# Performance work log

Hardware: AMD Instinct MI355X
Metric: run time of the kernel (lower is better)

Reference implementation:

```python
import jax, jax.numpy as jnp
import numpy as np

EMBED_DIM = 256
B, S = 4, 8192


def setup_inputs() -> dict:
    key = jax.random.key(0)
    ks = jax.random.split(key, 9)
    d = EMBED_DIM
    s = 1.0 / np.sqrt(d)
    return {
        "x": jax.random.normal(ks[0], (B, S, d), dtype=jnp.float32),
        "Wq": jax.random.uniform(ks[1], (d, d), jnp.float32, -s, s),
        "bq": jax.random.uniform(ks[2], (d,), jnp.float32, -s, s),
        "Wk": jax.random.uniform(ks[3], (d, d), jnp.float32, -s, s),
        "bk": jax.random.uniform(ks[4], (d,), jnp.float32, -s, s),
        "Wv": jax.random.uniform(ks[5], (d, d), jnp.float32, -s, s),
        "bv": jax.random.uniform(ks[6], (d,), jnp.float32, -s, s),
        "Wo": jax.random.uniform(ks[7], (d, d), jnp.float32, -s, s),
        "bo": jax.random.uniform(ks[8], (d,), jnp.float32, -s, s),
    }


def reference(x, Wq, bq, Wk, bk, Wv, bv, Wo, bo):
    # Linear layers: y = x @ W^T + b (torch convention: W is [out, in])
    d = x.shape[-1]
    scaling = d ** (-0.5)
    q = x @ Wq.T + bq                       # [B, S, d]
    k = x @ Wk.T + bk
    v = x @ Wv.T + bv
    scores = jnp.einsum("bsd,btd->bst", q, k) * scaling  # [B, S, S]
    weights = jax.nn.softmax(scores, axis=-1)
    attn = jnp.einsum("bst,btd->bsd", weights, v)        # [B, S, d]
    return attn @ Wo.T + bo
```

## Files before the change

### kernel.cpp

```cpp
#include <hip/hip_runtime.h>
#include <hip/hip_bf16.h>

typedef __attribute__((ext_vector_type(8))) short short8;
typedef __attribute__((ext_vector_type(4))) float f32x4;

#define SEQ 8192
#define NBATCH 4
#define NT (SEQ / 32)

static __device__ __forceinline__ unsigned short f2bf(float f) {
    __hip_bfloat16 h = __float2bfloat16(f);
    unsigned short u;
    __builtin_memcpy(&u, &h, 2);
    return u;
}

static __device__ __forceinline__ int4 pack8(float4 a, float4 b) {
    union { unsigned short s[8]; int4 i; } r;
    r.s[0] = f2bf(a.x); r.s[1] = f2bf(a.y); r.s[2] = f2bf(a.z); r.s[3] = f2bf(a.w);
    r.s[4] = f2bf(b.x); r.s[5] = f2bf(b.y); r.s[6] = f2bf(b.z); r.s[7] = f2bf(b.w);
    return r.i;
}

template<bool A_BF16, int OMODE>
__global__ __launch_bounds__(256) void proj_gemm(
    const void* __restrict__ Ap, const float* __restrict__ W,
    const float* __restrict__ bias, void* __restrict__ Outp, float scale)
{
    __shared__ alignas(16) unsigned short As[128][40];
    __shared__ alignas(16) unsigned short Bs[128][40];

    const int tid  = threadIdx.x;
    const int lane = tid & 63;
    const int wv   = tid >> 6;
    const int wm   = (wv >> 1) * 64, wn = (wv & 1) * 64;
    const int lr   = lane & 15, lg = lane >> 4;
    const int m0   = blockIdx.x * 128;
    const int n0   = blockIdx.y * 128;

    const int srow = tid >> 1;
    const int skc  = (tid & 1) * 16;

    f32x4 acc[4][4] = {};

    for (int k0 = 0; k0 < 256; k0 += 32) {
        __syncthreads();
        if (A_BF16) {
            const unsigned short* a = (const unsigned short*)Ap + (size_t)(m0 + srow) * 256 + k0 + skc;
            int4 v0 = *(const int4*)a;
            int4 v1 = *(const int4*)(a + 8);
            *(int4*)&As[srow][skc]     = v0;
            *(int4*)&As[srow][skc + 8] = v1;
        } else {
            const float* a = (const float*)Ap + (size_t)(m0 + srow) * 256 + k0 + skc;
            const float4* a4 = (const float4*)a;
            *(int4*)&As[srow][skc]     = pack8(a4[0], a4[1]);
            *(int4*)&As[srow][skc + 8] = pack8(a4[2], a4[3]);
        }
        {
            const float* b = W + (size_t)(n0 + srow) * 256 + k0 + skc;
            const float4* b4 = (const float4*)b;
            *(int4*)&Bs[srow][skc]     = pack8(b4[0], b4[1]);
            *(int4*)&Bs[srow][skc + 8] = pack8(b4[2], b4[3]);
        }
        __syncthreads();

        short8 af[4], bfr[4];
        #pragma unroll
        for (int fm = 0; fm < 4; ++fm)
            af[fm] = *(const short8*)&As[wm + fm * 16 + lr][lg * 8];
        #pragma unroll
        for (int fn = 0; fn < 4; ++fn)
            bfr[fn] = *(const short8*)&Bs[wn + fn * 16 + lr][lg * 8];
        #pragma unroll
        for (int fm = 0; fm < 4; ++fm)
            #pragma unroll
            for (int fn = 0; fn < 4; ++fn)
                acc[fm][fn] = __builtin_amdgcn_mfma_f32_16x16x32_bf16(
                    af[fm], bfr[fn], acc[fm][fn], 0, 0, 0);
    }

    float bvals[4];
    #pragma unroll
    for (int fn = 0; fn < 4; ++fn) bvals[fn] = bias[n0 + wn + fn * 16 + lr];

    #pragma unroll
    for (int fm = 0; fm < 4; ++fm) {
        #pragma unroll
        for (int fn = 0; fn < 4; ++fn) {
            #pragma unroll
            for (int r = 0; r < 4; ++r) {
                const int row = m0 + wm + fm * 16 + lg * 4 + r;
                const int col = n0 + wn + fn * 16 + lr;
                float val = (acc[fm][fn][r] + bvals[fn]) * scale;
                if (OMODE == 1) {
                    ((float*)Outp)[(size_t)row * 256 + col] = val;
                } else if (OMODE == 0) {
                    ((unsigned short*)Outp)[(size_t)row * 256 + col] = f2bf(val);
                } else {
                    const int bb = row >> 13, s = row & 8191;
                    ((unsigned short*)Outp)[((size_t)(bb * 256 + col) << 13) + s] = f2bf(val);
                }
            }
        }
    }
}

__global__ __launch_bounds__(256) void attn_kernel(
    const unsigned short* __restrict__ Q, const unsigned short* __restrict__ K,
    const unsigned short* __restrict__ Vt, unsigned short* __restrict__ A)
{
    __shared__ alignas(16) unsigned short Ks[2][32][264];
    __shared__ alignas(16) unsigned short Ps[2][4][16][40];
    __shared__ alignas(16) float Cor[2][4][16];
    __shared__ alignas(16) float Ls[4][16];
    __shared__ int Flg[2][4];

    const int tid  = threadIdx.x;
    const int lane = tid & 63;
    const int wv   = tid >> 6;
    const int lr   = lane & 15, lg = lane >> 4;
    const int b    = blockIdx.y;
    const size_t qblk = (size_t)b * SEQ + blockIdx.x * 64;

    short8 aq[8];
    #pragma unroll
    for (int c = 0; c < 8; ++c)
        aq[c] = *(const short8*)&Q[(qblk + wv * 16 + lr) * 256 + c * 32 + lg * 8];

    float m_run = -1e30f, l_run = 0.f;
    f32x4 o[4][4] = {};

    const int krow = tid >> 3, kcol = (tid & 7) * 32;
    const unsigned short* Vb = Vt + ((size_t)b * 256 << 13);
    size_t vrow[4];
    #pragma unroll
    for (int dt = 0; dt < 4; ++dt)
        vrow[dt] = (size_t)(wv * 64 + dt * 16 + lr) << 13;

    {
        const int4* src = (const int4*)&K[((size_t)b * SEQ + krow) * 256 + kcol];
        int4 x0 = src[0], x1 = src[1], x2 = src[2], x3 = src[3];
        *(int4*)&Ks[0][krow][kcol]      = x0;
        *(int4*)&Ks[0][krow][kcol + 8]  = x1;
        *(int4*)&Ks[0][krow][kcol + 16] = x2;
        *(int4*)&Ks[0][krow][kcol + 24] = x3;
    }
    __syncthreads();

    for (int it = 0; it < NT; ++it) {
        const int p = it & 1;
        int4 x0, x1, x2, x3;
        const bool have = (it + 1 < NT);
        if (have) {
            const int4* src = (const int4*)&K[((size_t)b * SEQ + (it + 1) * 32 + krow) * 256 + kcol];
            x0 = src[0]; x1 = src[1]; x2 = src[2]; x3 = src[3];
        }
        short8 vbr[4];
        if (it > 0) {
            const size_t kvp = (size_t)(it - 1) * 32 + lg * 8;
            #pragma unroll
            for (int dt = 0; dt < 4; ++dt)
                vbr[dt] = *(const short8*)&Vb[vrow[dt] + kvp];
        }

        f32x4 s0 = {}, s1 = {};
        #pragma unroll
        for (int c = 0; c < 8; ++c) {
            short8 kb0 = *(const short8*)&Ks[p][lr][c * 32 + lg * 8];
            short8 kb1 = *(const short8*)&Ks[p][16 + lr][c * 32 + lg * 8];
            s0 = __builtin_amdgcn_mfma_f32_16x16x32_bf16(kb0, aq[c], s0, 0, 0, 0);
            s1 = __builtin_amdgcn_mfma_f32_16x16x32_bf16(kb1, aq[c], s1, 0, 0, 0);
        }

        if (have) {
            *(int4*)&Ks[p ^ 1][krow][kcol]      = x0;
            *(int4*)&Ks[p ^ 1][krow][kcol + 8]  = x1;
            *(int4*)&Ks[p ^ 1][krow][kcol + 16] = x2;
            *(int4*)&Ks[p ^ 1][krow][kcol + 24] = x3;
        }

        float mx = fmaxf(fmaxf(fmaxf(s0[0], s0[1]), fmaxf(s0[2], s0[3])),
                         fmaxf(fmaxf(s1[0], s1[1]), fmaxf(s1[2], s1[3])));
        mx = fmaxf(mx, __shfl_xor(mx, 16, 64));
        mx = fmaxf(mx, __shfl_xor(mx, 32, 64));

        const int need = __any(mx > m_run + 11.0f);
        float corr = 1.f;
        if (need) {
            float mnew = fmaxf(m_run, mx);
            corr = exp2f(m_run - mnew);
            m_run = mnew;
            if (lane < 16) Cor[p ^ 1][wv][lr] = corr;
        }
        if (lane == 0) Flg[p ^ 1][wv] = need;

        float p0[4], p1[4];
        #pragma unroll
        for (int r = 0; r < 4; ++r) {
            p0[r] = exp2f(s0[r] - m_run);
            p1[r] = exp2f(s1[r] - m_run);
        }
        float rs = ((p0[0] + p0[1]) + (p0[2] + p0[3])) +
                   ((p1[0] + p1[1]) + (p1[2] + p1[3]));
        rs += __shfl_xor(rs, 16, 64);
        rs += __shfl_xor(rs, 32, 64);
        l_run = (need ? l_run * corr : l_run) + rs;

        {
            unsigned int w0 = (unsigned)f2bf(p0[0]) | ((unsigned)f2bf(p0[1]) << 16);
            unsigned int w1 = (unsigned)f2bf(p0[2]) | ((unsigned)f2bf(p0[3]) << 16);
            unsigned int w2 = (unsigned)f2bf(p1[0]) | ((unsigned)f2bf(p1[1]) << 16);
            unsigned int w3 = (unsigned)f2bf(p1[2]) | ((unsigned)f2bf(p1[3]) << 16);
            *(unsigned long long*)&Ps[p ^ 1][wv][lr][4 * lg] =
                (unsigned long long)w0 | ((unsigned long long)w1 << 32);
            *(unsigned long long*)&Ps[p ^ 1][wv][lr][16 + 4 * lg] =
                (unsigned long long)w2 | ((unsigned long long)w3 << 32);
        }

        if (it > 0) {
            short8 pa[4];
            #pragma unroll
            for (int qt = 0; qt < 4; ++qt)
                pa[qt] = *(const short8*)&Ps[p][qt][lr][lg * 8];
            #pragma unroll
            for (int qt = 0; qt < 4; ++qt) {
                if (Flg[p][qt]) {
                    float4 c4 = *(const float4*)&Cor[p][qt][lg * 4];
                    #pragma unroll
                    for (int dt = 0; dt < 4; ++dt) {
                        o[qt][dt][0] *= c4.x; o[qt][dt][1] *= c4.y;
                        o[qt][dt][2] *= c4.z; o[qt][dt][3] *= c4.w;
                    }
                }
                #pragma unroll
                for (int dt = 0; dt < 4; ++dt)
                    o[qt][dt] = __builtin_amdgcn_mfma_f32_16x16x32_bf16(pa[qt], vbr[dt], o[qt][dt], 0, 0, 0);
            }
        }
        __syncthreads();
    }

    {
        const int p = NT & 1;
        const size_t kvp = (size_t)(NT - 1) * 32 + lg * 8;
        short8 vbr[4];
        #pragma unroll
        for (int dt = 0; dt < 4; ++dt)
            vbr[dt] = *(const short8*)&Vb[vrow[dt] + kvp];
        short8 pa[4];
        #pragma unroll
        for (int qt = 0; qt < 4; ++qt)
            pa[qt] = *(const short8*)&Ps[p][qt][lr][lg * 8];
        #pragma unroll
        for (int qt = 0; qt < 4; ++qt) {
            if (Flg[p][qt]) {
                float4 c4 = *(const float4*)&Cor[p][qt][lg * 4];
                #pragma unroll
                for (int dt = 0; dt < 4; ++dt) {
                    o[qt][dt][0] *= c4.x; o[qt][dt][1] *= c4.y;
                    o[qt][dt][2] *= c4.z; o[qt][dt][3] *= c4.w;
                }
            }
            #pragma unroll
            for (int dt = 0; dt < 4; ++dt)
                o[qt][dt] = __builtin_amdgcn_mfma_f32_16x16x32_bf16(pa[qt], vbr[dt], o[qt][dt], 0, 0, 0);
        }
    }

    if (lane < 16) Ls[wv][lr] = l_run;
    __syncthreads();
    #pragma unroll
    for (int qt = 0; qt < 4; ++qt) {
        float4 l4 = *(const float4*)&Ls[qt][lg * 4];
        float inv[4] = {1.f / l4.x, 1.f / l4.y, 1.f / l4.z, 1.f / l4.w};
        #pragma unroll
        for (int dt = 0; dt < 4; ++dt)
            #pragma unroll
            for (int r = 0; r < 4; ++r)
                A[(qblk + qt * 16 + lg * 4 + r) * 256 + wv * 64 + dt * 16 + lr] =
                    f2bf(o[qt][dt][r] * inv[r]);
    }
}

extern "C" void kernel_launch(void* const* d_in, const int* in_sizes, int n_in,
                              void* d_out, int out_size, void* d_ws, size_t ws_size,
                              hipStream_t stream) {
    (void)in_sizes; (void)n_in; (void)out_size; (void)ws_size;
    const float* x  = (const float*)d_in[0];
    const float* Wq = (const float*)d_in[1];
    const float* bq = (const float*)d_in[2];
    const float* Wk = (const float*)d_in[3];
    const float* bk = (const float*)d_in[4];
    const float* Wv = (const float*)d_in[5];
    const float* bv = (const float*)d_in[6];
    const float* Wo = (const float*)d_in[7];
    const float* bo = (const float*)d_in[8];
    float* out = (float*)d_out;

    char* ws = (char*)d_ws;
    const size_t MB16 = (size_t)16 * 1024 * 1024;
    unsigned short* qb = (unsigned short*)(ws);
    unsigned short* kb = (unsigned short*)(ws + MB16);
    unsigned short* vt = (unsigned short*)(ws + 2 * MB16);
    unsigned short* ab = (unsigned short*)(ws + 3 * MB16);

    dim3 gg(256, 2), bb(256);
    proj_gemm<false, 0><<<gg, bb, 0, stream>>>(x, Wq, bq, qb, 0.0625f * 1.44269504f);
    proj_gemm<false, 0><<<gg, bb, 0, stream>>>(x, Wk, bk, kb, 1.0f);
    proj_gemm<false, 2><<<gg, bb, 0, stream>>>(x, Wv, bv, vt, 1.0f);
    attn_kernel<<<dim3(128, NBATCH), bb, 0, stream>>>(qb, kb, vt, ab);
    proj_gemm<true, 1><<<gg, bb, 0, stream>>>(ab, Wo, bo, out, 1.0f);
}
```

Measured before the change: 503.9 us.

## Load K fragments directly from global memory and drop the software pipeline

Removes the shared-memory double buffer for K tiles. Each wave now loads its K MFMA fragments straight from global memory, relying on L2/L1 since all four waves read the same tile. The one-iteration skew between QK^T and PV is also removed: PV for the current tile runs right after a barrier in the same iteration, which cuts LDS traffic and a prologue/epilogue. The cost is redundant global loads across waves and loss of latency hiding, since K and V loads now sit on the critical path of each iteration.

```diff
diff --git a/kernel.cpp b/kernel.cpp
--- a/kernel.cpp
+++ b/kernel.cpp
@@ -110,7 +110,6 @@
     const unsigned short* __restrict__ Q, const unsigned short* __restrict__ K,
     const unsigned short* __restrict__ Vt, unsigned short* __restrict__ A)
 {
-    __shared__ alignas(16) unsigned short Ks[2][32][264];
     __shared__ alignas(16) unsigned short Ps[2][4][16][40];
     __shared__ alignas(16) float Cor[2][4][16];
     __shared__ alignas(16) float Ls[4][16];
@@ -131,53 +130,37 @@
     float m_run = -1e30f, l_run = 0.f;
     f32x4 o[4][4] = {};
 
-    const int krow = tid >> 3, kcol = (tid & 7) * 32;
+    const unsigned short* Kb = K + (size_t)b * SEQ * 256;
     const unsigned short* Vb = Vt + ((size_t)b * 256 << 13);
     size_t vrow[4];
     #pragma unroll
     for (int dt = 0; dt < 4; ++dt)
         vrow[dt] = (size_t)(wv * 64 + dt * 16 + lr) << 13;
-
-    {
-        const int4* src = (const int4*)&K[((size_t)b * SEQ + krow) * 256 + kcol];
-        int4 x0 = src[0], x1 = src[1], x2 = src[2], x3 = src[3];
-        *(int4*)&Ks[0][krow][kcol]      = x0;
-        *(int4*)&Ks[0][krow][kcol + 8]  = x1;
-        *(int4*)&Ks[0][krow][kcol + 16] = x2;
-        *(int4*)&Ks[0][krow][kcol + 24] = x3;
-    }
-    __syncthreads();
+    const size_t krow0 = (size_t)lr * 256 + lg * 8;
+    const size_t krow1 = (size_t)(16 + lr) * 256 + lg * 8;
 
     for (int it = 0; it < NT; ++it) {
         const int p = it & 1;
-        int4 x0, x1, x2, x3;
-        const bool have = (it + 1 < NT);
-        if (have) {
-            const int4* src = (const int4*)&K[((size_t)b * SEQ + (it + 1) * 32 + krow) * 256 + kcol];
-            x0 = src[0]; x1 = src[1]; x2 = src[2]; x3 = src[3];
-        }
+        const unsigned short* Kt = Kb + (size_t)it * 32 * 256;
+
         short8 vbr[4];
-        if (it > 0) {
-            const size_t kvp = (size_t)(it - 1) * 32 + lg * 8;
-            #pragma unroll
-            for (int dt = 0; dt < 4; ++dt)
-                vbr[dt] = *(const short8*)&Vb[vrow[dt] + kvp];
+        const size_t kvp = (size_t)it * 32 + lg * 8;
+        #pragma unroll
+        for (int dt = 0; dt < 4; ++dt)
+            vbr[dt] = *(const short8*)&Vb[vrow[dt] + kvp];
+
+        short8 kf0[8], kf1[8];
+        #pragma unroll
+        for (int c = 0; c < 8; ++c) {
+            kf0[c] = *(const short8*)&Kt[krow0 + c * 32];
+            kf1[c] = *(const short8*)&Kt[krow1 + c * 32];
         }
 
         f32x4 s0 = {}, s1 = {};
         #pragma unroll
         for (int c = 0; c < 8; ++c) {
-            short8 kb0 = *(const short8*)&Ks[p][lr][c * 32 + lg * 8];
-            short8 kb1 = *(const short8*)&Ks[p][16 + lr][c * 32 + lg * 8];
-            s0 = __builtin_amdgcn_mfma_f32_16x16x32_bf16(kb0, aq[c], s0, 0, 0, 0);
-            s1 = __builtin_amdgcn_mfma_f32_16x16x32_bf16(kb1, aq[c], s1, 0, 0, 0);
-        }
-
-        if (have) {
-            *(int4*)&Ks[p ^ 1][krow][kcol]      = x0;
-            *(int4*)&Ks[p ^ 1][krow][kcol + 8]  = x1;
-            *(int4*)&Ks[p ^ 1][krow][kcol + 16] = x2;
-            *(int4*)&Ks[p ^ 1][krow][kcol + 24] = x3;
+            s0 = __builtin_amdgcn_mfma_f32_16x16x32_bf16(kf0[c], aq[c], s0, 0, 0, 0);
+            s1 = __builtin_amdgcn_mfma_f32_16x16x32_bf16(kf1[c], aq[c], s1, 0, 0, 0);
         }
 
         float mx = fmaxf(fmaxf(fmaxf(s0[0], s0[1]), fmaxf(s0[2], s0[3])),
@@ -191,9 +174,9 @@
             float mnew = fmaxf(m_run, mx);
             corr = exp2f(m_run - mnew);
             m_run = mnew;
-            if (lane < 16) Cor[p ^ 1][wv][lr] = corr;
-        }
-        if (lane == 0) Flg[p ^ 1][wv] = need;
+            if (lane < 16) Cor[p][wv][lr] = corr;
+        }
+        if (lane == 0) Flg[p][wv] = need;
 
         float p0[4], p1[4];
         #pragma unroll
@@ -212,42 +195,13 @@
             unsigned int w1 = (unsigned)f2bf(p0[2]) | ((unsigned)f2bf(p0[3]) << 16);
             unsigned int w2 = (unsigned)f2bf(p1[0]) | ((unsigned)f2bf(p1[1]) << 16);
             unsigned int w3 = (unsigned)f2bf(p1[2]) | ((unsigned)f2bf(p1[3]) << 16);
-            *(unsigned long long*)&Ps[p ^ 1][wv][lr][4 * lg] =
+            *(unsigned long long*)&Ps[p][wv][lr][4 * lg] =
                 (unsigned long long)w0 | ((unsigned long long)w1 << 32);
-            *(unsigned long long*)&Ps[p ^ 1][wv][lr][16 + 4 * lg] =
+            *(unsigned long long*)&Ps[p][wv][lr][16 + 4 * lg] =
                 (unsigned long long)w2 | ((unsigned long long)w3 << 32);
         }
-
-        if (it > 0) {
-            short8 pa[4];
-            #pragma unroll
-            for (int qt = 0; qt < 4; ++qt)
-                pa[qt] = *(const short8*)&Ps[p][qt][lr][lg * 8];
-            #pragma unroll
-            for (int qt = 0; qt < 4; ++qt) {
-                if (Flg[p][qt]) {
-                    float4 c4 = *(const float4*)&Cor[p][qt][lg * 4];
-                    #pragma unroll
-                    for (int dt = 0; dt < 4; ++dt) {
-                        o[qt][dt][0] *= c4.x; o[qt][dt][1] *= c4.y;
-                        o[qt][dt][2] *= c4.z; o[qt][dt][3] *= c4.w;
-                    }
-                }
-                #pragma unroll
-                for (int dt = 0; dt < 4; ++dt)
-                    o[qt][dt] = __builtin_amdgcn_mfma_f32_16x16x32_bf16(pa[qt], vbr[dt], o[qt][dt], 0, 0, 0);
-            }
-        }
         __syncthreads();
-    }
-
-    {
-        const int p = NT & 1;
-        const size_t kvp = (size_t)(NT - 1) * 32 + lg * 8;
-        short8 vbr[4];
-        #pragma unroll
-        for (int dt = 0; dt < 4; ++dt)
-            vbr[dt] = *(const short8*)&Vb[vrow[dt] + kvp];
+
         short8 pa[4];
         #pragma unroll
         for (int qt = 0; qt < 4; ++qt)
```

Result: slower. 1.183 ms (+134.7%).

## Double query rows per attention block to reuse K/V tiles across 128 queries

Applied to the files above, without the earlier changes.

Each attention workgroup now handles 128 query rows instead of 64, with each wave owning two 16-row query tiles, so every K tile in shared memory and every V fragment from global memory serves twice as many queries. The P·V MFMA for the previous tile is moved ahead of the softmax of the current tile to overlap it with score work. This halves the grid to 256 blocks and roughly doubles accumulator registers per thread (launch bounds set to 1 block), trading occupancy and CU fill on a large GPU for less K/V traffic.

```diff
diff --git a/kernel.cpp b/kernel.cpp
--- a/kernel.cpp
+++ b/kernel.cpp
@@ -106,32 +106,36 @@
     }
 }
 
-__global__ __launch_bounds__(256) void attn_kernel(
+__global__ __launch_bounds__(256, 1) void attn_kernel(
     const unsigned short* __restrict__ Q, const unsigned short* __restrict__ K,
     const unsigned short* __restrict__ Vt, unsigned short* __restrict__ A)
 {
     __shared__ alignas(16) unsigned short Ks[2][32][264];
-    __shared__ alignas(16) unsigned short Ps[2][4][16][40];
-    __shared__ alignas(16) float Cor[2][4][16];
-    __shared__ alignas(16) float Ls[4][16];
-    __shared__ int Flg[2][4];
+    __shared__ alignas(16) unsigned short Ps[2][8][16][40];
+    __shared__ alignas(16) float Cor[2][128];
+    __shared__ alignas(16) float Ls[128];
+    __shared__ int Flg[2][8];
 
     const int tid  = threadIdx.x;
     const int lane = tid & 63;
     const int wv   = tid >> 6;
     const int lr   = lane & 15, lg = lane >> 4;
     const int b    = blockIdx.y;
-    const size_t qblk = (size_t)b * SEQ + blockIdx.x * 64;
-
-    short8 aq[8];
-    #pragma unroll
-    for (int c = 0; c < 8; ++c)
-        aq[c] = *(const short8*)&Q[(qblk + wv * 16 + lr) * 256 + c * 32 + lg * 8];
-
-    float m_run = -1e30f, l_run = 0.f;
-    f32x4 o[4][4] = {};
+    const size_t qblk = (size_t)b * SEQ + blockIdx.x * 128;
+
+    short8 aq0[8], aq1[8];
+    #pragma unroll
+    for (int c = 0; c < 8; ++c) {
+        aq0[c] = *(const short8*)&Q[(qblk + wv * 32 + lr) * 256 + c * 32 + lg * 8];
+        aq1[c] = *(const short8*)&Q[(qblk + wv * 32 + 16 + lr) * 256 + c * 32 + lg * 8];
+    }
+
+    float m0 = -1e30f, l0 = 0.f;
+    float m1 = -1e30f, l1 = 0.f;
+    f32x4 o[8][4] = {};
 
     const int krow = tid >> 3, kcol = (tid & 7) * 32;
+    const unsigned short* Kb = K + (size_t)b * SEQ * 256;
     const unsigned short* Vb = Vt + ((size_t)b * 256 << 13);
     size_t vrow[4];
     #pragma unroll
@@ -139,7 +143,7 @@
         vrow[dt] = (size_t)(wv * 64 + dt * 16 + lr) << 13;
 
     {
-        const int4* src = (const int4*)&K[((size_t)b * SEQ + krow) * 256 + kcol];
+        const int4* src = (const int4*)&Kb[(size_t)krow * 256 + kcol];
         int4 x0 = src[0], x1 = src[1], x2 = src[2], x3 = src[3];
         *(int4*)&Ks[0][krow][kcol]      = x0;
         *(int4*)&Ks[0][krow][kcol + 8]  = x1;
@@ -148,85 +152,44 @@
     }
     __syncthreads();
 
-    for (int it = 0; it < NT; ++it) {
-        const int p = it & 1;
+    for (int t = 0; t < NT; ++t) {
+        const int p = t & 1;
+        const bool have = (t + 1 < NT);
+
         int4 x0, x1, x2, x3;
-        const bool have = (it + 1 < NT);
         if (have) {
-            const int4* src = (const int4*)&K[((size_t)b * SEQ + (it + 1) * 32 + krow) * 256 + kcol];
+            const int4* src = (const int4*)&Kb[((size_t)(t + 1) * 32 + krow) * 256 + kcol];
             x0 = src[0]; x1 = src[1]; x2 = src[2]; x3 = src[3];
         }
         short8 vbr[4];
-        if (it > 0) {
-            const size_t kvp = (size_t)(it - 1) * 32 + lg * 8;
+        if (t > 0) {
+            const size_t kvp = (size_t)(t - 1) * 32 + lg * 8;
             #pragma unroll
             for (int dt = 0; dt < 4; ++dt)
                 vbr[dt] = *(const short8*)&Vb[vrow[dt] + kvp];
         }
 
-        f32x4 s0 = {}, s1 = {};
+        f32x4 s00 = {}, s01 = {}, s10 = {}, s11 = {};
         #pragma unroll
         for (int c = 0; c < 8; ++c) {
             short8 kb0 = *(const short8*)&Ks[p][lr][c * 32 + lg * 8];
             short8 kb1 = *(const short8*)&Ks[p][16 + lr][c * 32 + lg * 8];
-            s0 = __builtin_amdgcn_mfma_f32_16x16x32_bf16(kb0, aq[c], s0, 0, 0, 0);
-            s1 = __builtin_amdgcn_mfma_f32_16x16x32_bf16(kb1, aq[c], s1, 0, 0, 0);
-        }
-
-        if (have) {
-            *(int4*)&Ks[p ^ 1][krow][kcol]      = x0;
-            *(int4*)&Ks[p ^ 1][krow][kcol + 8]  = x1;
-            *(int4*)&Ks[p ^ 1][krow][kcol + 16] = x2;
-            *(int4*)&Ks[p ^ 1][krow][kcol + 24] = x3;
-        }
-
-        float mx = fmaxf(fmaxf(fmaxf(s0[0], s0[1]), fmaxf(s0[2], s0[3])),
-                         fmaxf(fmaxf(s1[0], s1[1]), fmaxf(s1[2], s1[3])));
-        mx = fmaxf(mx, __shfl_xor(mx, 16, 64));
-        mx = fmaxf(mx, __shfl_xor(mx, 32, 64));
-
-        const int need = __any(mx > m_run + 11.0f);
-        float corr = 1.f;
-        if (need) {
-            float mnew = fmaxf(m_run, mx);
-            corr = exp2f(m_run - mnew);
-            m_run = mnew;
-            if (lane < 16) Cor[p ^ 1][wv][lr] = corr;
-        }
-        if (lane == 0) Flg[p ^ 1][wv] = need;
-
-        float p0[4], p1[4];
-        #pragma unroll
-        for (int r = 0; r < 4; ++r) {
-            p0[r] = exp2f(s0[r] - m_run);
-            p1[r] = exp2f(s1[r] - m_run);
-        }
-        float rs = ((p0[0] + p0[1]) + (p0[2] + p0[3])) +
-                   ((p1[0] + p1[1]) + (p1[2] + p1[3]));
-        rs += __shfl_xor(rs, 16, 64);
-        rs += __shfl_xor(rs, 32, 64);
-        l_run = (need ? l_run * corr : l_run) + rs;
-
-        {
-            unsigned int w0 = (unsigned)f2bf(p0[0]) | ((unsigned)f2bf(p0[1]) << 16);
-            unsigned int w1 = (unsigned)f2bf(p0[2]) | ((unsigned)f2bf(p0[3]) << 16);
-            unsigned int w2 = (unsigned)f2bf(p1[0]) | ((unsigned)f2bf(p1[1]) << 16);
-            unsigned int w3 = (unsigned)f2bf(p1[2]) | ((unsigned)f2bf(p1[3]) << 16);
-            *(unsigned long long*)&Ps[p ^ 1][wv][lr][4 * lg] =
-                (unsigned long long)w0 | ((unsigned long long)w1 << 32);
-            *(unsigned long long*)&Ps[p ^ 1][wv][lr][16 + 4 * lg] =
-                (unsigned long long)w2 | ((unsigned long long)w3 << 32);
-        }
-
-        if (it > 0) {
-            short8 pa[4];
-            #pragma unroll
-            for (int qt = 0; qt < 4; ++qt)
-                pa[qt] = *(const short8*)&Ps[p][qt][lr][lg * 8];
-            #pragma unroll
-            for (int qt = 0; qt < 4; ++qt) {
-                if (Flg[p][qt]) {
-                    float4 c4 = *(const float4*)&Cor[p][qt][lg * 4];
+            s00 = __builtin_amdgcn_mfma_f32_16x16x32_bf16(kb0, aq0[c], s00, 0, 0, 0);
+            s01 = __builtin_amdgcn_mfma_f32_16x16x32_bf16(kb1, aq0[c], s01, 0, 0, 0);
+            s10 = __builtin_amdgcn_mfma_f32_16x16x32_bf16(kb0, aq1[c], s10, 0, 0, 0);
+            s11 = __builtin_amdgcn_mfma_f32_16x16x32_bf16(kb1, aq1[c], s11, 0, 0, 0);
+        }
+
+        if (t > 0) {
+            const int q = p ^ 1;
+            short8 pa[8];
+            #pragma unroll
+            for (int qt = 0; qt < 8; ++qt)
+                pa[qt] = *(const short8*)&Ps[q][qt][lr][lg * 8];
+            #pragma unroll
+            for (int qt = 0; qt < 8; ++qt) {
+                if (Flg[q][qt]) {
+                    float4 c4 = *(const float4*)&Cor[q][qt * 16 + lg * 4];
                     #pragma unroll
                     for (int dt = 0; dt < 4; ++dt) {
                         o[qt][dt][0] *= c4.x; o[qt][dt][1] *= c4.y;
@@ -238,24 +201,88 @@
                     o[qt][dt] = __builtin_amdgcn_mfma_f32_16x16x32_bf16(pa[qt], vbr[dt], o[qt][dt], 0, 0, 0);
             }
         }
+
+        float mx0 = fmaxf(fmaxf(fmaxf(s00[0], s00[1]), fmaxf(s00[2], s00[3])),
+                          fmaxf(fmaxf(s01[0], s01[1]), fmaxf(s01[2], s01[3])));
+        float mx1 = fmaxf(fmaxf(fmaxf(s10[0], s10[1]), fmaxf(s10[2], s10[3])),
+                          fmaxf(fmaxf(s11[0], s11[1]), fmaxf(s11[2], s11[3])));
+        mx0 = fmaxf(mx0, __shfl_xor(mx0, 16, 64));
+        mx0 = fmaxf(mx0, __shfl_xor(mx0, 32, 64));
+        mx1 = fmaxf(mx1, __shfl_xor(mx1, 16, 64));
+        mx1 = fmaxf(mx1, __shfl_xor(mx1, 32, 64));
+
+        const int need = __any((mx0 > m0 + 11.0f) || (mx1 > m1 + 11.0f));
+        if (need) {
+            float n0 = fmaxf(m0, mx0), n1 = fmaxf(m1, mx1);
+            float c0 = exp2f(m0 - n0), c1 = exp2f(m1 - n1);
+            m0 = n0; m1 = n1;
+            if (lane < 16) {
+                Cor[p][wv * 32 + lr]      = c0;
+                Cor[p][wv * 32 + 16 + lr] = c1;
+            }
+            if (need) { l0 *= c0; l1 *= c1; }
+        }
+        if (lane == 0) { Flg[p][2 * wv] = need; Flg[p][2 * wv + 1] = need; }
+
+        float pa0[4], pb0[4], pa1[4], pb1[4];
+        #pragma unroll
+        for (int r = 0; r < 4; ++r) {
+            pa0[r] = exp2f(s00[r] - m0);
+            pb0[r] = exp2f(s01[r] - m0);
+            pa1[r] = exp2f(s10[r] - m1);
+            pb1[r] = exp2f(s11[r] - m1);
+        }
+        float rs0 = ((pa0[0] + pa0[1]) + (pa0[2] + pa0[3])) +
+                    ((pb0[0] + pb0[1]) + (pb0[2] + pb0[3]));
+        float rs1 = ((pa1[0] + pa1[1]) + (pa1[2] + pa1[3])) +
+                    ((pb1[0] + pb1[1]) + (pb1[2] + pb1[3]));
+        rs0 += __shfl_xor(rs0, 16, 64); rs0 += __shfl_xor(rs0, 32, 64);
+        rs1 += __shfl_xor(rs1, 16, 64); rs1 += __shfl_xor(rs1, 32, 64);
+        l0 += rs0; l1 += rs1;
+
+        {
+            unsigned int w0 = (unsigned)f2bf(pa0[0]) | ((unsigned)f2bf(pa0[1]) << 16);
+            unsigned int w1 = (unsigned)f2bf(pa0[2]) | ((unsigned)f2bf(pa0[3]) << 16);
+            unsigned int w2 = (unsigned)f2bf(pb0[0]) | ((unsigned)f2bf(pb0[1]) << 16);
+            unsigned int w3 = (unsigned)f2bf(pb0[2]) | ((unsigned)f2bf(pb0[3]) << 16);
+            *(unsigned long long*)&Ps[p][2 * wv][lr][4 * lg] =
+                (unsigned long long)w0 | ((unsigned long long)w1 << 32);
+            *(unsigned long long*)&Ps[p][2 * wv][lr][16 + 4 * lg] =
+                (unsigned long long)w2 | ((unsigned long long)w3 << 32);
+            unsigned int w4 = (unsigned)f2bf(pa1[0]) | ((unsigned)f2bf(pa1[1]) << 16);
+            unsigned int w5 = (unsigned)f2bf(pa1[2]) | ((unsigned)f2bf(pa1[3]) << 16);
+            unsigned int w6 = (unsigned)f2bf(pb1[0]) | ((unsigned)f2bf(pb1[1]) << 16);
+            unsigned int w7 = (unsigned)f2bf(pb1[2]) | ((unsigned)f2bf(pb1[3]) << 16);
+            *(unsigned long long*)&Ps[p][2 * wv + 1][lr][4 * lg] =
+                (unsigned long long)w4 | ((unsigned long long)w5 << 32);
+            *(unsigned long long*)&Ps[p][2 * wv + 1][lr][16 + 4 * lg] =
+                (unsigned long long)w6 | ((unsigned long long)w7 << 32);
+        }
+
+        if (have) {
+            *(int4*)&Ks[p ^ 1][krow][kcol]      = x0;
+            *(int4*)&Ks[p ^ 1][krow][kcol + 8]  = x1;
+            *(int4*)&Ks[p ^ 1][krow][kcol + 16] = x2;
+            *(int4*)&Ks[p ^ 1][krow][kcol + 24] = x3;
+        }
         __syncthreads();
     }
 
     {
-        const int p = NT & 1;
+        const int q = (NT - 1) & 1;
         const size_t kvp = (size_t)(NT - 1) * 32 + lg * 8;
         short8 vbr[4];
         #pragma unroll
         for (int dt = 0; dt < 4; ++dt)
             vbr[dt] = *(const short8*)&Vb[vrow[dt] + kvp];
-        short8 pa[4];
-        #pragma unroll
-        for (int qt = 0; qt < 4; ++qt)
-            pa[qt] = *(const short8*)&Ps[p][qt][lr][lg * 8];
-        #pragma unroll
-        for (int qt = 0; qt < 4; ++qt) {
-            if (Flg[p][qt]) {
-                float4 c4 = *(const float4*)&Cor[p][qt][lg * 4];
+        short8 pa[8];
+        #pragma unroll
+        for (int qt = 0; qt < 8; ++qt)
+            pa[qt] = *(const short8*)&Ps[q][qt][lr][lg * 8];
+        #pragma unroll
+        for (int qt = 0; qt < 8; ++qt) {
+            if (Flg[q][qt]) {
+                float4 c4 = *(const float4*)&Cor[q][qt * 16 + lg * 4];
                 #pragma unroll
                 for (int dt = 0; dt < 4; ++dt) {
                     o[qt][dt][0] *= c4.x; o[qt][dt][1] *= c4.y;
@@ -268,11 +295,11 @@
         }
     }
 
-    if (lane < 16) Ls[wv][lr] = l_run;
+    if (lane < 16) { Ls[wv * 32 + lr] = l0; Ls[wv * 32 + 16 + lr] = l1; }
     __syncthreads();
     #pragma unroll
-    for (int qt = 0; qt < 4; ++qt) {
-        float4 l4 = *(const float4*)&Ls[qt][lg * 4];
+    for (int qt = 0; qt < 8; ++qt) {
+        float4 l4 = *(const float4*)&Ls[qt * 16 + lg * 4];
         float inv[4] = {1.f / l4.x, 1.f / l4.y, 1.f / l4.z, 1.f / l4.w};
         #pragma unroll
         for (int dt = 0; dt < 4; ++dt)
@@ -309,6 +336,6 @@
     proj_gemm<false, 0><<<gg, bb, 0, stream>>>(x, Wq, bq, qb, 0.0625f * 1.44269504f);
     proj_gemm<false, 0><<<gg, bb, 0, stream>>>(x, Wk, bk, kb, 1.0f);
     proj_gemm<false, 2><<<gg, bb, 0, stream>>>(x, Wv, bv, vt, 1.0f);
-    attn_kernel<<<dim3(128, NBATCH), bb, 0, stream>>>(qb, kb, vt, ab);
+    attn_kernel<<<dim3(64, NBATCH), bb, 0, stream>>>(qb, kb, vt, ab);
     proj_gemm<true, 1><<<gg, bb, 0, stream>>>(ab, Wo, bo, out, 1.0f);
 }
```

Result: slower. 676.8 us (+34.3%).

## Load K tiles directly into LDS with global_load_lds and padded layout

Applied to the files above, without the earlier changes.

Replaces the register-staged K tile prefetch (global load into registers, then LDS store after the QK MFMAs) with asynchronous global_load_lds writes straight into the next LDS buffer. The LDS layout becomes row pairs with 1040-byte pitch so each wave's 64-lane load of two rows lands contiguously, and the read offsets are changed to match. This is meant to save VGPRs and remove the LDS store instructions from the loop. The risk is that the async loads must be complete before the next iteration reads them, and the existing barrier may not wait on them correctly.

```diff
diff --git a/kernel.cpp b/kernel.cpp
--- a/kernel.cpp
+++ b/kernel.cpp
@@ -106,11 +106,13 @@
     }
 }
 
+#define KROWOFF(r) (((r) >> 1) * 1040 + ((r) & 1) * 512)
+
 __global__ __launch_bounds__(256) void attn_kernel(
     const unsigned short* __restrict__ Q, const unsigned short* __restrict__ K,
     const unsigned short* __restrict__ Vt, unsigned short* __restrict__ A)
 {
-    __shared__ alignas(16) unsigned short Ks[2][32][264];
+    __shared__ alignas(16) char Ks[2][16640];
     __shared__ alignas(16) unsigned short Ps[2][4][16][40];
     __shared__ alignas(16) float Cor[2][4][16];
     __shared__ alignas(16) float Ls[4][16];
@@ -131,34 +133,45 @@
     float m_run = -1e30f, l_run = 0.f;
     f32x4 o[4][4] = {};
 
-    const int krow = tid >> 3, kcol = (tid & 7) * 32;
+    const unsigned short* Kb = K + (size_t)b * SEQ * 256;
     const unsigned short* Vb = Vt + ((size_t)b * 256 << 13);
     size_t vrow[4];
     #pragma unroll
     for (int dt = 0; dt < 4; ++dt)
         vrow[dt] = (size_t)(wv * 64 + dt * 16 + lr) << 13;
 
-    {
-        const int4* src = (const int4*)&K[((size_t)b * SEQ + krow) * 256 + kcol];
-        int4 x0 = src[0], x1 = src[1], x2 = src[2], x3 = src[3];
-        *(int4*)&Ks[0][krow][kcol]      = x0;
-        *(int4*)&Ks[0][krow][kcol + 8]  = x1;
-        *(int4*)&Ks[0][krow][kcol + 16] = x2;
-        *(int4*)&Ks[0][krow][kcol + 24] = x3;
+    const int srow = lane >> 5;
+    const int scol = (lane & 31) * 8;
+    const int kb_base = KROWOFF(lr) + lg * 16;
+
+    #pragma unroll
+    for (int i = 0; i < 4; ++i) {
+        const int pr = 4 * wv + i;
+        const unsigned short* src = Kb + (size_t)(2 * pr + srow) * 256 + scol;
+        __builtin_amdgcn_global_load_lds(
+            (const __attribute__((address_space(1))) void*)src,
+            (__attribute__((address_space(3))) void*)&Ks[0][pr * 1040], 16, 0, 0);
     }
     __syncthreads();
 
-    for (int it = 0; it < NT; ++it) {
-        const int p = it & 1;
-        int4 x0, x1, x2, x3;
-        const bool have = (it + 1 < NT);
-        if (have) {
-            const int4* src = (const int4*)&K[((size_t)b * SEQ + (it + 1) * 32 + krow) * 256 + kcol];
-            x0 = src[0]; x1 = src[1]; x2 = src[2]; x3 = src[3];
-        }
+    for (int t = 0; t < NT; ++t) {
+        const int p = t & 1;
+
+        if (t + 1 < NT) {
+            #pragma unroll
+            for (int i = 0; i < 4; ++i) {
+                const int pr = 4 * wv + i;
+                const unsigned short* src =
+                    Kb + ((size_t)(t + 1) * 32 + 2 * pr + srow) * 256 + scol;
+                __builtin_amdgcn_global_load_lds(
+                    (const __attribute__((address_space(1))) void*)src,
+                    (__attribute__((address_space(3))) void*)&Ks[p ^ 1][pr * 1040], 16, 0, 0);
+            }
+        }
+
         short8 vbr[4];
-        if (it > 0) {
-            const size_t kvp = (size_t)(it - 1) * 32 + lg * 8;
+        if (t > 0) {
+            const size_t kvp = (size_t)(t - 1) * 32 + lg * 8;
             #pragma unroll
             for (int dt = 0; dt < 4; ++dt)
                 vbr[dt] = *(const short8*)&Vb[vrow[dt] + kvp];
@@ -167,17 +180,10 @@
         f32x4 s0 = {}, s1 = {};
         #pragma unroll
         for (int c = 0; c < 8; ++c) {
-            short8 kb0 = *(const short8*)&Ks[p][lr][c * 32 + lg * 8];
-            short8 kb1 = *(const short8*)&Ks[p][16 + lr][c * 32 + lg * 8];
+            short8 kb0 = *(const short8*)&Ks[p][kb_base + c * 64];
+            short8 kb1 = *(const short8*)&Ks[p][kb_base + 8320 + c * 64];
             s0 = __builtin_amdgcn_mfma_f32_16x16x32_bf16(kb0, aq[c], s0, 0, 0, 0);
             s1 = __builtin_amdgcn_mfma_f32_16x16x32_bf16(kb1, aq[c], s1, 0, 0, 0);
-        }
-
-        if (have) {
-            *(int4*)&Ks[p ^ 1][krow][kcol]      = x0;
-            *(int4*)&Ks[p ^ 1][krow][kcol + 8]  = x1;
-            *(int4*)&Ks[p ^ 1][krow][kcol + 16] = x2;
-            *(int4*)&Ks[p ^ 1][krow][kcol + 24] = x3;
         }
 
         float mx = fmaxf(fmaxf(fmaxf(s0[0], s0[1]), fmaxf(s0[2], s0[3])),
@@ -218,7 +224,7 @@
                 (unsigned long long)w2 | ((unsigned long long)w3 << 32);
         }
 
-        if (it > 0) {
+        if (t > 0) {
             short8 pa[4];
             #pragma unroll
             for (int qt = 0; qt < 4; ++qt)
```

Result: slower. 557.2 us (+10.6%).
